# Optimization experiments

Measured on AMD Instinct MI355X. Metric: run time of the kernel, lower is better.

The kernel has to match this reference:

```python
import jax, jax.numpy as jnp
import numpy as np

N_NODES = 50000
N_EDGES = 800000
IN_DIM = 128
EDGE_DIM = 16
HIDDEN = 128
N_LAYERS = 3
N_GRAPHS = 256
BN_EPS = 1e-5


def setup_inputs() -> dict:
    key = jax.random.key(0)
    ks = jax.random.split(key, 24)
    s = 0.05
    inp = {
        "x": jax.random.normal(ks[0], (N_NODES, IN_DIM), jnp.float32),
        "edge_index": jax.random.randint(ks[1], (2, N_EDGES), 0, N_NODES, jnp.int32),
        "edge_attr": jax.random.normal(ks[2], (N_EDGES, EDGE_DIM), jnp.float32),
        "batch": jnp.sort(jax.random.randint(ks[3], (N_NODES,), 0, N_GRAPHS, jnp.int32)),
        "n_graphs": N_GRAPHS,
        # input projection
        "lin_in_w": jax.random.normal(ks[4], (IN_DIM, HIDDEN), jnp.float32) * s,
        "lin_in_b": jnp.zeros((HIDDEN,), jnp.float32),
        # per-layer message MLP (stacked over layers)
        "msg_w1": jax.random.normal(ks[5], (N_LAYERS, HIDDEN + EDGE_DIM, HIDDEN), jnp.float32) * s,
        "msg_b1": jnp.zeros((N_LAYERS, HIDDEN), jnp.float32),
        "msg_w2": jax.random.normal(ks[6], (N_LAYERS, HIDDEN, HIDDEN), jnp.float32) * s,
        "msg_b2": jnp.zeros((N_LAYERS, HIDDEN), jnp.float32),
        # BatchNorm (eval mode: running stats)
        "bn_gamma": jnp.ones((N_LAYERS, HIDDEN), jnp.float32),
        "bn_beta": jnp.zeros((N_LAYERS, HIDDEN), jnp.float32),
        "bn_mean": jax.random.normal(ks[7], (N_LAYERS, HIDDEN), jnp.float32) * 0.01,
        "bn_var": jax.random.uniform(ks[8], (N_LAYERS, HIDDEN), jnp.float32, 0.5, 1.5),
        # GRUCell params (PyTorch layout: [3*H, H], gate order r,z,n)
        "gru_wih": jax.random.normal(ks[9], (N_LAYERS, 3 * HIDDEN, HIDDEN), jnp.float32) * s,
        "gru_whh": jax.random.normal(ks[10], (N_LAYERS, 3 * HIDDEN, HIDDEN), jnp.float32) * s,
        "gru_bih": jnp.zeros((N_LAYERS, 3 * HIDDEN), jnp.float32),
        "gru_bhh": jnp.zeros((N_LAYERS, 3 * HIDDEN), jnp.float32),
        # readout linear: [2H -> H]
        "ro_w": jax.random.normal(ks[11], (2 * HIDDEN, HIDDEN), jnp.float32) * s,
        "ro_b": jnp.zeros((HIDDEN,), jnp.float32),
    }
    return inp


def _gru_cell(x, h, wih, whh, bih, bhh):
    gi = x @ wih.T + bih  # [N, 3H]
    gh = h @ whh.T + bhh
    ir, iz, inn = jnp.split(gi, 3, axis=1)
    hr, hz, hn = jnp.split(gh, 3, axis=1)
    r = jax.nn.sigmoid(ir + hr)
    z = jax.nn.sigmoid(iz + hz)
    n = jnp.tanh(inn + r * hn)
    return (1.0 - z) * n + z * h


def reference(x, edge_index, edge_attr, batch, n_graphs,
              lin_in_w, lin_in_b, msg_w1, msg_b1, msg_w2, msg_b2,
              bn_gamma, bn_beta, bn_mean, bn_var,
              gru_wih, gru_whh, gru_bih, gru_bhh, ro_w, ro_b):
    h = jax.nn.relu(x @ lin_in_w + lin_in_b)  # [N, H]
    src, dst = edge_index[0], edge_index[1]
    n_nodes = h.shape[0]
    for l in range(N_LAYERS):
        m_in = jnp.concatenate([h[src], edge_attr], axis=1)  # [E, H+Ed]
        m = jax.nn.relu(m_in @ msg_w1[l] + msg_b1[l]) @ msg_w2[l] + msg_b2[l]  # [E, H]
        agg = jax.ops.segment_sum(m, dst, num_segments=n_nodes)  # scatter-add
        h_new = _gru_cell(agg, h, gru_wih[l], gru_whh[l], gru_bih[l], gru_bhh[l])
        bn = (h_new - bn_mean[l]) * jax.lax.rsqrt(bn_var[l] + BN_EPS) * bn_gamma[l] + bn_beta[l]
        h = h + bn  # dropout is identity in eval mode
    # readout: segment mean + segment max over graphs
    cnt = jax.ops.segment_sum(jnp.ones((n_nodes, 1), h.dtype), batch, num_segments=n_graphs)
    z_sum = jax.ops.segment_sum(h, batch, num_segments=n_graphs)
    z_mean = z_sum / jnp.maximum(cnt, 1.0)
    z_max = jax.ops.segment_max(h, batch, num_segments=n_graphs)
    z_max = jnp.where(cnt > 0, z_max, 0.0)  # empty graphs -> 0 (as in torch code)
    z = jax.nn.relu(jnp.concatenate([z_mean, z_max], axis=1) @ ro_w + ro_b)
    return z
```

## Files before the change

### kernel.cpp

```cpp
#include <hip/hip_runtime.h>
#include <math.h>

constexpr int NN = 50000;
constexpr int NE = 800000;
constexpr int H  = 128;
constexpr int ED = 16;
constexpr int NL = 3;
constexpr int NG = 256;
constexpr int NBINS = 50176;

typedef __attribute__((ext_vector_type(8))) short bf8;
typedef __attribute__((ext_vector_type(4))) float f32x4;

__device__ __forceinline__ unsigned short f2bf(float f) {
    unsigned u = __float_as_uint(f);
    unsigned r = (u + 0x7FFFu + ((u >> 16) & 1u)) >> 16;
    return (unsigned short)r;
}
__device__ __forceinline__ float bf2f(unsigned short b) {
    return __uint_as_float(((unsigned)b) << 16);
}

__global__ __launch_bounds__(256) void k_zero4(float4* __restrict__ a, int n4) {
    int i = blockIdx.x * 256 + threadIdx.x;
    if (i < n4) a[i] = make_float4(0.f, 0.f, 0.f, 0.f);
}

__global__ __launch_bounds__(256) void k_sort_zero(int* __restrict__ counts) {
    int i = blockIdx.x * 256 + threadIdx.x;
    counts[i] = 0;
}

__global__ __launch_bounds__(256) void k_hist(const int* __restrict__ ei,
                                              int* __restrict__ counts) {
    int e = blockIdx.x * 256 + threadIdx.x;
    if (e < NE) atomicAdd(&counts[ei[NE + e]], 1);
}

__global__ __launch_bounds__(256) void k_scan1(const int* __restrict__ counts,
                                               int* __restrict__ incl,
                                               int* __restrict__ bsum) {
    __shared__ int s[256];
    int t = threadIdx.x;
    int i = blockIdx.x * 256 + t;
    int v = counts[i];
    s[t] = v;
    __syncthreads();
    #pragma unroll
    for (int off = 1; off < 256; off <<= 1) {
        int x = (t >= off) ? s[t - off] : 0;
        __syncthreads();
        s[t] += x;
        __syncthreads();
    }
    incl[i] = s[t];
    if (t == 255) bsum[blockIdx.x] = s[255];
}

__global__ __launch_bounds__(256) void k_scan2(int* __restrict__ bsum) {
    __shared__ int s[256];
    int t = threadIdx.x;
    int v = (t < 196) ? bsum[t] : 0;
    s[t] = v;
    __syncthreads();
    #pragma unroll
    for (int off = 1; off < 256; off <<= 1) {
        int x = (t >= off) ? s[t - off] : 0;
        __syncthreads();
        s[t] += x;
        __syncthreads();
    }
    if (t < 196) bsum[t] = s[t] - v;
}

__global__ __launch_bounds__(256) void k_scan3(const int* __restrict__ counts,
                                               const int* __restrict__ incl,
                                               const int* __restrict__ bsum,
                                               int* __restrict__ cur) {
    int i = blockIdx.x * 256 + threadIdx.x;
    cur[i] = incl[i] - counts[i] + bsum[blockIdx.x];
}

__global__ __launch_bounds__(256) void k_scatter_perm(const int* __restrict__ ei,
                                                      int* __restrict__ cur,
                                                      int* __restrict__ perm) {
    int e = blockIdx.x * 256 + threadIdx.x;
    if (e < NE) {
        int d = ei[NE + e];
        int pos = atomicAdd(&cur[d], 1);
        perm[pos] = e;
    }
}

__global__ __launch_bounds__(256) void k_prep(const float* __restrict__ wih,
                                              const float* __restrict__ whh,
                                              const float* __restrict__ w1,
                                              const float* __restrict__ w2,
                                              const float* __restrict__ lin_w,
                                              unsigned short* __restrict__ wgru,
                                              unsigned short* __restrict__ w1et,
                                              unsigned short* __restrict__ w2t,
                                              unsigned short* __restrict__ w1ht,
                                              unsigned short* __restrict__ winT) {
    int i = blockIdx.x * 256 + threadIdx.x;
    if (i < 294912) {
        int m = i / 147456, rem = i % 147456;
        wgru[i] = f2bf((m == 0 ? wih : whh)[rem]);
        return;
    }
    i -= 294912;
    if (i < NL * 128 * 32) {
        int l = i / 4096, rem = i % 4096;
        int n = rem >> 5, k = rem & 31;
        float v = (k < ED) ? w1[(size_t)l * 144 * 128 + (size_t)(128 + k) * 128 + n] : 0.f;
        w1et[i] = f2bf(v);
        return;
    }
    i -= NL * 128 * 32;
    if (i < NL * 128 * 128) {
        int l = i / 16384, rem = i % 16384;
        int n = rem >> 7, k = rem & 127;
        w2t[i] = f2bf(w2[(size_t)l * 16384 + (size_t)k * 128 + n]);
        return;
    }
    i -= NL * 128 * 128;
    if (i < NL * 128 * 128) {
        int l = i / 16384, rem = i % 16384;
        int n = rem >> 7, k = rem & 127;
        w1ht[i] = f2bf(w1[(size_t)l * 144 * 128 + (size_t)k * 128 + n]);
        return;
    }
    i -= NL * 128 * 128;
    if (i < 128 * 128) {
        int n = i >> 7, k = i & 127;
        winT[i] = f2bf(lin_w[k * 128 + n]);
    }
}

template <bool A_F32, bool RELU, bool BIAS, bool OUT_F32>
__global__ __launch_bounds__(256) void k_mfma_gemm(const float* __restrict__ A_f,
                                                   const unsigned short* __restrict__ A_bf,
                                                   const unsigned short* __restrict__ Bt,
                                                   const float* __restrict__ bias,
                                                   float* __restrict__ C_f,
                                                   unsigned short* __restrict__ C_bf,
                                                   int M) {
    __shared__ unsigned short As[32][136];
    const int t = threadIdx.x;
    const int w = t >> 6, lane = t & 63, l15 = lane & 15, q = lane >> 4;
    const int n0 = blockIdx.x * 32;

    bf8 bfr[2][4];
    #pragma unroll
    for (int nt = 0; nt < 2; ++nt) {
        int n = w * 32 + nt * 16 + l15;
        #pragma unroll
        for (int ks = 0; ks < 4; ++ks)
            bfr[nt][ks] = *(const bf8*)(Bt + (size_t)n * 128 + ks * 32 + q * 8);
    }

    {
        int r = t >> 3, cs = (t & 7) * 16;
        int row = n0 + r;
        union { uint4 u[2]; unsigned short s[16]; } pk;
        if (A_F32) {
            float4 v[4];
            if (row < M) {
                const float4* src = (const float4*)(A_f + (size_t)row * H + cs);
                v[0] = src[0]; v[1] = src[1]; v[2] = src[2]; v[3] = src[3];
            } else {
                v[0] = v[1] = v[2] = v[3] = make_float4(0.f, 0.f, 0.f, 0.f);
            }
            #pragma unroll
            for (int j = 0; j < 4; ++j) {
                pk.s[j * 4 + 0] = f2bf(v[j].x); pk.s[j * 4 + 1] = f2bf(v[j].y);
                pk.s[j * 4 + 2] = f2bf(v[j].z); pk.s[j * 4 + 3] = f2bf(v[j].w);
            }
        } else {
            if (row < M) {
                const uint4* src = (const uint4*)(A_bf + (size_t)row * H + cs);
                pk.u[0] = src[0]; pk.u[1] = src[1];
            } else {
                pk.u[0] = pk.u[1] = make_uint4(0, 0, 0, 0);
            }
        }
        *(uint4*)&As[r][cs] = pk.u[0];
        *(uint4*)&As[r][cs + 8] = pk.u[1];
    }
    __syncthreads();

    f32x4 acc[2][2];
    #pragma unroll
    for (int mt = 0; mt < 2; ++mt)
        #pragma unroll
        for (int nt = 0; nt < 2; ++nt) acc[mt][nt] = {0.f, 0.f, 0.f, 0.f};

    #pragma unroll
    for (int ks = 0; ks < 4; ++ks) {
        #pragma unroll
        for (int mt = 0; mt < 2; ++mt) {
            bf8 af = *(const bf8*)&As[mt * 16 + l15][ks * 32 + q * 8];
            acc[mt][0] = __builtin_amdgcn_mfma_f32_16x16x32_bf16(af, bfr[0][ks], acc[mt][0], 0, 0, 0);
            acc[mt][1] = __builtin_amdgcn_mfma_f32_16x16x32_bf16(af, bfr[1][ks], acc[mt][1], 0, 0, 0);
        }
    }

    #pragma unroll
    for (int nt = 0; nt < 2; ++nt) {
        int col = w * 32 + nt * 16 + l15;
        float bv = BIAS ? bias[col] : 0.f;
        #pragma unroll
        for (int mt = 0; mt < 2; ++mt) {
            #pragma unroll
            for (int r = 0; r < 4; ++r) {
                int node = n0 + mt * 16 + q * 4 + r;
                if (node < M) {
                    float v = acc[mt][nt][r] + bv;
                    if (RELU) v = fmaxf(v, 0.f);
                    if (OUT_F32) C_f[(size_t)node * H + col] = v;
                    C_bf[(size_t)node * H + col] = f2bf(v);
                }
            }
        }
    }
}

__global__ __launch_bounds__(256, 4) void k_edge_mfma(
        const unsigned short* __restrict__ p,
        const float* __restrict__ ea,
        const int* __restrict__ ei,
        const int* __restrict__ perm,
        const unsigned short* __restrict__ w1et,
        const float* __restrict__ b1,
        const unsigned short* __restrict__ w2t,
        const float* __restrict__ b2,
        float* __restrict__ agg) {
    __shared__ unsigned short hid_s[64][136];
    __shared__ unsigned short pm_s[64][136];
    __shared__ int src_s[64], dst_s[64], perm_s[64];

    const int t    = threadIdx.x;
    const int w    = t >> 6;
    const int lane = t & 63;
    const int l15  = lane & 15;
    const int q    = lane >> 4;

    bf8 w1f[2];
    bf8 w2f[2][4];
    float b1v[2], b2v[2];
    #pragma unroll
    for (int nt = 0; nt < 2; ++nt) {
        int n = w * 32 + nt * 16 + l15;
        w1f[nt] = *(const bf8*)(w1et + (size_t)n * 32 + q * 8);
        #pragma unroll
        for (int ks = 0; ks < 4; ++ks)
            w2f[nt][ks] = *(const bf8*)(w2t + (size_t)n * 128 + ks * 32 + q * 8);
        b1v[nt] = b1[n];
        b2v[nt] = b2[n];
    }

    const f32x4 zero = {0.f, 0.f, 0.f, 0.f};

    for (int base = blockIdx.x * 64; base < NE; base += gridDim.x * 64) {
        if (t < 64) {
            int e = perm[base + t];
            perm_s[t] = e;
            src_s[t]  = ei[e];
            dst_s[t]  = ei[NE + e];
        }
        __syncthreads();

        {
            int row = t >> 4, seg = t & 15;
            #pragma unroll
            for (int it = 0; it < 4; ++it, row += 16)
                *(uint4*)&pm_s[row][seg * 8] =
                    *(const uint4*)(p + (size_t)src_s[row] * H + seg * 8);
        }

        f32x4 acc1[4][2];
        #pragma unroll
        for (int mt = 0; mt < 4; ++mt) {
            bf8 af = {0, 0, 0, 0, 0, 0, 0, 0};
            if (q < 2) {
                int e = perm_s[mt * 16 + l15];
                const float4* e4 = (const float4*)(ea + (size_t)e * ED + q * 8);
                float4 v0 = e4[0], v1 = e4[1];
                af[0] = (short)f2bf(v0.x); af[1] = (short)f2bf(v0.y);
                af[2] = (short)f2bf(v0.z); af[3] = (short)f2bf(v0.w);
                af[4] = (short)f2bf(v1.x); af[5] = (short)f2bf(v1.y);
                af[6] = (short)f2bf(v1.z); af[7] = (short)f2bf(v1.w);
            }
            #pragma unroll
            for (int nt = 0; nt < 2; ++nt)
                acc1[mt][nt] = __builtin_amdgcn_mfma_f32_16x16x32_bf16(af, w1f[nt], zero, 0, 0, 0);
        }
        __syncthreads();

        #pragma unroll
        for (int mt = 0; mt < 4; ++mt) {
            #pragma unroll
            for (int r = 0; r < 4; ++r) {
                int er = mt * 16 + q * 4 + r;
                #pragma unroll
                for (int nt = 0; nt < 2; ++nt) {
                    int col = w * 32 + nt * 16 + l15;
                    float v = acc1[mt][nt][r] + bf2f(pm_s[er][col]) + b1v[nt];
                    hid_s[er][col] = f2bf(fmaxf(v, 0.f));
                }
            }
        }
        __syncthreads();

        f32x4 acc2[4][2];
        #pragma unroll
        for (int mt = 0; mt < 4; ++mt)
            #pragma unroll
            for (int nt = 0; nt < 2; ++nt) acc2[mt][nt] = zero;

        #pragma unroll
        for (int ks = 0; ks < 4; ++ks) {
            #pragma unroll
            for (int mt = 0; mt < 4; ++mt) {
                bf8 af = *(const bf8*)&hid_s[mt * 16 + l15][ks * 32 + q * 8];
                acc2[mt][0] = __builtin_amdgcn_mfma_f32_16x16x32_bf16(af, w2f[0][ks], acc2[mt][0], 0, 0, 0);
                acc2[mt][1] = __builtin_amdgcn_mfma_f32_16x16x32_bf16(af, w2f[1][ks], acc2[mt][1], 0, 0, 0);
            }
        }
        #pragma unroll
        for (int mt = 0; mt < 4; ++mt) {
            #pragma unroll
            for (int r = 0; r < 4; ++r) {
                int er = mt * 16 + q * 4 + r;
                #pragma unroll
                for (int nt = 0; nt < 2; ++nt) {
                    int col = w * 32 + nt * 16 + l15;
                    pm_s[er][col] = f2bf(acc2[mt][nt][r] + b2v[nt]);
                }
            }
        }
        __syncthreads();

        {
            int c = t & 127, hh = t >> 7;
            float sum = 0.f;
            int prev = dst_s[hh * 32];
            #pragma unroll 4
            for (int i = 0; i < 32; ++i) {
                int e = hh * 32 + i;
                int d = dst_s[e];
                float v = bf2f(pm_s[e][c]);
                if (d != prev) {
                    atomicAdd(&agg[(size_t)prev * H + c], sum);
                    sum = 0.f;
                    prev = d;
                }
                sum += v;
            }
            atomicAdd(&agg[(size_t)prev * H + c], sum);
        }
        __syncthreads();
    }
}

__device__ __forceinline__ float sigmoidf_(float x) { return 1.f / (1.f + expf(-x)); }

__global__ __launch_bounds__(256) void k_gru_mfma(const float* __restrict__ agg,
                                                  float* __restrict__ h,
                                                  unsigned short* __restrict__ h_bf,
                                                  const unsigned short* __restrict__ wih,
                                                  const unsigned short* __restrict__ whh,
                                                  const float* __restrict__ bih,
                                                  const float* __restrict__ bhh,
                                                  const float* __restrict__ gamma,
                                                  const float* __restrict__ beta,
                                                  const float* __restrict__ mean,
                                                  const float* __restrict__ var) {
    __shared__ unsigned short ab[32][136];
    __shared__ unsigned short hb[32][136];
    __shared__ float hf[32][132];
    const int t = threadIdx.x;
    const int w = t >> 6, lane = t & 63, l15 = lane & 15, q = lane >> 4;
    const int n0 = blockIdx.x * 32;

    {
        int r = t >> 3, cs = (t & 7) * 16;
        int row = n0 + r;
        float4 va[4], vh[4];
        if (row < NN) {
            const float4* sa = (const float4*)(agg + (size_t)row * H + cs);
            const float4* sh = (const float4*)(h + (size_t)row * H + cs);
            #pragma unroll
            for (int j = 0; j < 4; ++j) { va[j] = sa[j]; vh[j] = sh[j]; }
        } else {
            #pragma unroll
            for (int j = 0; j < 4; ++j) {
                va[j] = make_float4(0.f, 0.f, 0.f, 0.f);
                vh[j] = va[j];
            }
        }
        union { uint4 u[2]; unsigned short s[16]; } pa, ph;
        #pragma unroll
        for (int j = 0; j < 4; ++j) {
            pa.s[j * 4 + 0] = f2bf(va[j].x); pa.s[j * 4 + 1] = f2bf(va[j].y);
            pa.s[j * 4 + 2] = f2bf(va[j].z); pa.s[j * 4 + 3] = f2bf(va[j].w);
            ph.s[j * 4 + 0] = f2bf(vh[j].x); ph.s[j * 4 + 1] = f2bf(vh[j].y);
            ph.s[j * 4 + 2] = f2bf(vh[j].z); ph.s[j * 4 + 3] = f2bf(vh[j].w);
            *(float4*)&hf[r][cs + j * 4] = vh[j];
        }
        *(uint4*)&ab[r][cs] = pa.u[0];  *(uint4*)&ab[r][cs + 8] = pa.u[1];
        *(uint4*)&hb[r][cs] = ph.u[0];  *(uint4*)&hb[r][cs + 8] = ph.u[1];
    }
    __syncthreads();

    f32x4 acc[2][2][3][2];
    #pragma unroll
    for (int mt = 0; mt < 2; ++mt)
        #pragma unroll
        for (int io = 0; io < 2; ++io)
            #pragma unroll
            for (int g = 0; g < 3; ++g)
                #pragma unroll
                for (int nt = 0; nt < 2; ++nt) acc[mt][io][g][nt] = {0.f, 0.f, 0.f, 0.f};

    #pragma unroll
    for (int ks = 0; ks < 4; ++ks) {
        bf8 a_a[2], a_h[2];
        #pragma unroll
        for (int mt = 0; mt < 2; ++mt) {
            a_a[mt] = *(const bf8*)&ab[mt * 16 + l15][ks * 32 + q * 8];
            a_h[mt] = *(const bf8*)&hb[mt * 16 + l15][ks * 32 + q * 8];
        }
        #pragma unroll
        for (int g = 0; g < 3; ++g) {
            #pragma unroll
            for (int nt = 0; nt < 2; ++nt) {
                int n = g * 128 + w * 32 + nt * 16 + l15;
                bf8 bi = *(const bf8*)(wih + (size_t)n * 128 + ks * 32 + q * 8);
                bf8 bh = *(const bf8*)(whh + (size_t)n * 128 + ks * 32 + q * 8);
                #pragma unroll
                for (int mt = 0; mt < 2; ++mt) {
                    acc[mt][0][g][nt] = __builtin_amdgcn_mfma_f32_16x16x32_bf16(a_a[mt], bi, acc[mt][0][g][nt], 0, 0, 0);
                    acc[mt][1][g][nt] = __builtin_amdgcn_mfma_f32_16x16x32_bf16(a_h[mt], bh, acc[mt][1][g][nt], 0, 0, 0);
                }
            }
        }
    }

    #pragma unroll
    for (int nt = 0; nt < 2; ++nt) {
        int col = w * 32 + nt * 16 + l15;
        float bir = bih[col], biz = bih[128 + col], bin = bih[256 + col];
        float bhr = bhh[col], bhz = bhh[128 + col], bhn = bhh[256 + col];
        float ga = gamma[col], be = beta[col], mu = mean[col];
        float iv = rsqrtf(var[col] + 1e-5f);
        #pragma unroll
        for (int mt = 0; mt < 2; ++mt) {
            #pragma unroll
            for (int r = 0; r < 4; ++r) {
                int nl = mt * 16 + q * 4 + r;
                int node = n0 + nl;
                if (node < NN) {
                    float ir = acc[mt][0][0][nt][r] + bir;
                    float iz = acc[mt][0][1][nt][r] + biz;
                    float in = acc[mt][0][2][nt][r] + bin;
                    float hr = acc[mt][1][0][nt][r] + bhr;
                    float hz = acc[mt][1][1][nt][r] + bhz;
                    float hn = acc[mt][1][2][nt][r] + bhn;
                    float rg = sigmoidf_(ir + hr);
                    float zg = sigmoidf_(iz + hz);
                    float ng = tanhf(in + rg * hn);
                    float hv = hf[nl][col];
                    float hnew = (1.f - zg) * ng + zg * hv;
                    float bn = (hnew - mu) * iv * ga + be;
                    float out = hv + bn;
                    h[(size_t)node * H + col] = out;
                    h_bf[(size_t)node * H + col] = f2bf(out);
                }
            }
        }
    }
}

__device__ __forceinline__ unsigned fkey(float f) {
    unsigned b = __float_as_uint(f);
    return (b & 0x80000000u) ? ~b : (b | 0x80000000u);
}
__device__ __forceinline__ float funkey(unsigned k) {
    unsigned b = (k & 0x80000000u) ? (k & 0x7FFFFFFFu) : ~k;
    return __uint_as_float(b);
}

__global__ __launch_bounds__(256) void k_ro_init(float* __restrict__ gsum,
                                                 unsigned* __restrict__ gmaxb,
                                                 float* __restrict__ gcnt) {
    int i = blockIdx.x * 256 + threadIdx.x;
    if (i < NG * H) { gsum[i] = 0.f; gmaxb[i] = 0u; }
    if (i < NG) gcnt[i] = 0.f;
}

__global__ __launch_bounds__(256) void k_ro_scan(const float* __restrict__ h,
                                                 const int* __restrict__ batch,
                                                 float* __restrict__ gsum,
                                                 unsigned* __restrict__ gmaxb,
                                                 float* __restrict__ gcnt) {
    __shared__ int bt_s[64];
    const int t = threadIdx.x;
    const int n0 = blockIdx.x * 64;
    if (t < 64) bt_s[t] = (n0 + t < NN) ? batch[n0 + t] : -1;
    __syncthreads();

    int c = t & 127, hh = t >> 7;
    float sum = 0.f, mx = -3.4e38f, cnt = 0.f;
    int prev = bt_s[hh * 32];
    #pragma unroll 4
    for (int i = 0; i < 32; ++i) {
        int e = hh * 32 + i;
        int g = bt_s[e];
        if (g != prev) {
            if (prev >= 0) {
                atomicAdd(&gsum[prev * H + c], sum);
                atomicMax(&gmaxb[prev * H + c], fkey(mx));
                if (c == 0) atomicAdd(&gcnt[prev], cnt);
            }
            sum = 0.f; mx = -3.4e38f; cnt = 0.f;
            prev = g;
        }
        if (g >= 0) {
            float v = h[(size_t)(n0 + e) * H + c];
            sum += v;
            mx = fmaxf(mx, v);
            cnt += 1.f;
        }
    }
    if (prev >= 0) {
        atomicAdd(&gsum[prev * H + c], sum);
        atomicMax(&gmaxb[prev * H + c], fkey(mx));
        if (c == 0) atomicAdd(&gcnt[prev], cnt);
    }
}

__global__ __launch_bounds__(128) void k_ro_final(const float* __restrict__ gsum,
                                                  const unsigned* __restrict__ gmaxb,
                                                  const float* __restrict__ gcnt,
                                                  const float* __restrict__ row,
                                                  const float* __restrict__ rob,
                                                  float* __restrict__ out) {
    __shared__ float cat[256];
    const int g = blockIdx.x, t = threadIdx.x;
    float cnt = gcnt[g];
    float inv = 1.f / fmaxf(cnt, 1.f);
    cat[t] = gsum[g * H + t] * inv;
    float mx = funkey(gmaxb[g * H + t]);
    cat[128 + t] = (cnt > 0.f) ? mx : 0.f;
    __syncthreads();
    float acc = rob[t];
    #pragma unroll 4
    for (int k = 0; k < 256; ++k) acc += cat[k] * row[k * H + t];
    out[g * H + t] = fmaxf(acc, 0.f);
}

extern "C" void kernel_launch(void* const* d_in, const int* in_sizes, int n_in,
                              void* d_out, int out_size, void* d_ws, size_t ws_size,
                              hipStream_t stream) {
    const float* x        = (const float*)d_in[0];
    const int*   ei       = (const int*)d_in[1];
    const float* ea       = (const float*)d_in[2];
    const int*   batch    = (const int*)d_in[3];
    const float* lin_in_w = (const float*)d_in[5];
    const float* lin_in_b = (const float*)d_in[6];
    const float* msg_w1   = (const float*)d_in[7];
    const float* msg_b1   = (const float*)d_in[8];
    const float* msg_w2   = (const float*)d_in[9];
    const float* msg_b2   = (const float*)d_in[10];
    const float* bn_gamma = (const float*)d_in[11];
    const float* bn_beta  = (const float*)d_in[12];
    const float* bn_mean  = (const float*)d_in[13];
    const float* bn_var   = (const float*)d_in[14];
    const float* gru_wih  = (const float*)d_in[15];
    const float* gru_whh  = (const float*)d_in[16];
    const float* gru_bih  = (const float*)d_in[17];
    const float* gru_bhh  = (const float*)d_in[18];
    const float* ro_w     = (const float*)d_in[19];
    const float* ro_b     = (const float*)d_in[20];

    float* ws = (float*)d_ws;
    float*          h     = ws;
    float*          agg   = ws + 6400000;
    unsigned short* h_bf  = (unsigned short*)(ws + 12800000);
    unsigned short* p_bf  = (unsigned short*)(ws + 16000000);
    float*          gsum  = ws + 19200000;
    unsigned*       gmaxb = (unsigned*)(ws + 19232768);
    float*          gcnt  = ws + 19265536;
    unsigned short* wgru  = (unsigned short*)(ws + 19265792);
    unsigned short* w1et  = (unsigned short*)(ws + 19413248);
    unsigned short* w2t   = (unsigned short*)(ws + 19419392);
    unsigned short* w1ht  = (unsigned short*)(ws + 19443968);
    unsigned short* winT  = (unsigned short*)(ws + 19468544);
    int*            cnts  = (int*)(ws + 19476736);
    int*            incl  = (int*)(ws + 19526912);
    int*            cur   = (int*)(ws + 19577088);
    int*            bsum  = (int*)(ws + 19627264);
    int*            perm  = (int*)(ws + 19627520);

    k_prep<<<1648, 256, 0, stream>>>(gru_wih, gru_whh, msg_w1, msg_w2, lin_in_w,
                                     wgru, w1et, w2t, w1ht, winT);

    k_sort_zero<<<196, 256, 0, stream>>>(cnts);
    k_hist<<<3125, 256, 0, stream>>>(ei, cnts);
    k_scan1<<<196, 256, 0, stream>>>(cnts, incl, bsum);
    k_scan2<<<1, 256, 0, stream>>>(bsum);
    k_scan3<<<196, 256, 0, stream>>>(cnts, incl, bsum, cur);
    k_scatter_perm<<<3125, 256, 0, stream>>>(ei, cur, perm);

    k_mfma_gemm<true, true, true, true><<<1563, 256, 0, stream>>>(
        x, nullptr, winT, lin_in_b, h, h_bf, NN);

    for (int l = 0; l < NL; ++l) {
        k_mfma_gemm<false, false, false, false><<<1563, 256, 0, stream>>>(
            nullptr, h_bf, w1ht + (size_t)l * 16384, nullptr, nullptr, p_bf, NN);
        k_zero4<<<6250, 256, 0, stream>>>((float4*)agg, 1600000);
        k_edge_mfma<<<1024, 256, 0, stream>>>(p_bf, ea, ei, perm,
                                              w1et + (size_t)l * 4096, msg_b1 + l * 128,
                                              w2t + (size_t)l * 16384, msg_b2 + l * 128,
                                              agg);
        k_gru_mfma<<<1563, 256, 0, stream>>>(agg, h, h_bf,
                                             wgru + (size_t)l * 49152,
                                             wgru + (size_t)(NL + l) * 49152,
                                             gru_bih + l * 384, gru_bhh + l * 384,
                                             bn_gamma + l * 128, bn_beta + l * 128,
                                             bn_mean + l * 128, bn_var + l * 128);
    }

    k_ro_init<<<128, 256, 0, stream>>>(gsum, gmaxb, gcnt);
    k_ro_scan<<<782, 256, 0, stream>>>(h, batch, gsum, gmaxb, gcnt);
    k_ro_final<<<NG, 128, 0, stream>>>(gsum, gmaxb, gcnt, ro_w, ro_b, (float*)d_out);
}
```

Baseline: 862.9 us.

## Pre-gather sorted src/dst and bf16 edge attrs; shrink edge kernel LDS

Adds a one-time gather that writes src and dst indices plus bf16 edge attributes in dst-sorted order. The per-layer edge kernel then reads them contiguously instead of doing indirect perm lookups and fp32 conversion. The edge kernel reuses a single LDS buffer (with an extra barrier), which allows higher occupancy (launch bounds 6, more blocks). It also drops the bf16 copy of h, so the GEMM converts from fp32 itself, and replaces the zeroing kernels with hipMemsetAsync. The cost is an extra preprocessing pass and one more sync per tile.

```diff
diff --git a/kernel.cpp b/kernel.cpp
--- a/kernel.cpp
+++ b/kernel.cpp
@@ -7,7 +7,6 @@
 constexpr int ED = 16;
 constexpr int NL = 3;
 constexpr int NG = 256;
-constexpr int NBINS = 50176;
 
 typedef __attribute__((ext_vector_type(8))) short bf8;
 typedef __attribute__((ext_vector_type(4))) float f32x4;
@@ -19,11 +18,6 @@
 }
 __device__ __forceinline__ float bf2f(unsigned short b) {
     return __uint_as_float(((unsigned)b) << 16);
-}
-
-__global__ __launch_bounds__(256) void k_zero4(float4* __restrict__ a, int n4) {
-    int i = blockIdx.x * 256 + threadIdx.x;
-    if (i < n4) a[i] = make_float4(0.f, 0.f, 0.f, 0.f);
 }
 
 __global__ __launch_bounds__(256) void k_sort_zero(int* __restrict__ counts) {
@@ -90,6 +84,31 @@
         int pos = atomicAdd(&cur[d], 1);
         perm[pos] = e;
     }
+}
+
+__global__ __launch_bounds__(256) void k_gather(const int* __restrict__ ei,
+                                                const float* __restrict__ ea,
+                                                int* __restrict__ perm,
+                                                int* __restrict__ dsts,
+                                                unsigned short* __restrict__ ea_bf) {
+    int i = blockIdx.x * 256 + threadIdx.x;
+    if (i >= NE) return;
+    int e = perm[i];
+    perm[i] = ei[e];
+    dsts[i] = ei[NE + e];
+    const float4* s = (const float4*)(ea + (size_t)e * ED);
+    float4 v[4];
+    #pragma unroll
+    for (int j = 0; j < 4; ++j) v[j] = s[j];
+    union { uint4 u[2]; unsigned short sh[16]; } pk;
+    #pragma unroll
+    for (int j = 0; j < 4; ++j) {
+        pk.sh[j * 4 + 0] = f2bf(v[j].x); pk.sh[j * 4 + 1] = f2bf(v[j].y);
+        pk.sh[j * 4 + 2] = f2bf(v[j].z); pk.sh[j * 4 + 3] = f2bf(v[j].w);
+    }
+    uint4* d = (uint4*)(ea_bf + (size_t)i * 16);
+    d[0] = pk.u[0];
+    d[1] = pk.u[1];
 }
 
 __global__ __launch_bounds__(256) void k_prep(const float* __restrict__ wih,
@@ -137,9 +156,8 @@
     }
 }
 
-template <bool A_F32, bool RELU, bool BIAS, bool OUT_F32>
-__global__ __launch_bounds__(256) void k_mfma_gemm(const float* __restrict__ A_f,
-                                                   const unsigned short* __restrict__ A_bf,
+template <bool RELU, bool BIAS, bool OUT_F32, bool OUT_BF>
+__global__ __launch_bounds__(256) void k_mfma_gemm(const float* __restrict__ A,
                                                    const unsigned short* __restrict__ Bt,
                                                    const float* __restrict__ bias,
                                                    float* __restrict__ C_f,
@@ -162,27 +180,20 @@
     {
         int r = t >> 3, cs = (t & 7) * 16;
         int row = n0 + r;
+        float4 v[4];
+        if (row < M) {
+            const float4* src = (const float4*)(A + (size_t)row * H + cs);
+            #pragma unroll
+            for (int j = 0; j < 4; ++j) v[j] = src[j];
+        } else {
+            #pragma unroll
+            for (int j = 0; j < 4; ++j) v[j] = make_float4(0.f, 0.f, 0.f, 0.f);
+        }
         union { uint4 u[2]; unsigned short s[16]; } pk;
-        if (A_F32) {
-            float4 v[4];
-            if (row < M) {
-                const float4* src = (const float4*)(A_f + (size_t)row * H + cs);
-                v[0] = src[0]; v[1] = src[1]; v[2] = src[2]; v[3] = src[3];
-            } else {
-                v[0] = v[1] = v[2] = v[3] = make_float4(0.f, 0.f, 0.f, 0.f);
-            }
-            #pragma unroll
-            for (int j = 0; j < 4; ++j) {
-                pk.s[j * 4 + 0] = f2bf(v[j].x); pk.s[j * 4 + 1] = f2bf(v[j].y);
-                pk.s[j * 4 + 2] = f2bf(v[j].z); pk.s[j * 4 + 3] = f2bf(v[j].w);
-            }
-        } else {
-            if (row < M) {
-                const uint4* src = (const uint4*)(A_bf + (size_t)row * H + cs);
-                pk.u[0] = src[0]; pk.u[1] = src[1];
-            } else {
-                pk.u[0] = pk.u[1] = make_uint4(0, 0, 0, 0);
-            }
+        #pragma unroll
+        for (int j = 0; j < 4; ++j) {
+            pk.s[j * 4 + 0] = f2bf(v[j].x); pk.s[j * 4 + 1] = f2bf(v[j].y);
+            pk.s[j * 4 + 2] = f2bf(v[j].z); pk.s[j * 4 + 3] = f2bf(v[j].w);
         }
         *(uint4*)&As[r][cs] = pk.u[0];
         *(uint4*)&As[r][cs + 8] = pk.u[1];
@@ -218,26 +229,25 @@
                     float v = acc[mt][nt][r] + bv;
                     if (RELU) v = fmaxf(v, 0.f);
                     if (OUT_F32) C_f[(size_t)node * H + col] = v;
-                    C_bf[(size_t)node * H + col] = f2bf(v);
+                    if (OUT_BF)  C_bf[(size_t)node * H + col] = f2bf(v);
                 }
             }
         }
     }
 }
 
-__global__ __launch_bounds__(256, 4) void k_edge_mfma(
+__global__ __launch_bounds__(256, 6) void k_edge_mfma(
         const unsigned short* __restrict__ p,
-        const float* __restrict__ ea,
-        const int* __restrict__ ei,
-        const int* __restrict__ perm,
+        const int* __restrict__ srcs,
+        const int* __restrict__ dsts,
+        const unsigned short* __restrict__ ea_bf,
         const unsigned short* __restrict__ w1et,
         const float* __restrict__ b1,
         const unsigned short* __restrict__ w2t,
         const float* __restrict__ b2,
         float* __restrict__ agg) {
-    __shared__ unsigned short hid_s[64][136];
-    __shared__ unsigned short pm_s[64][136];
-    __shared__ int src_s[64], dst_s[64], perm_s[64];
+    __shared__ unsigned short u_s[64][136];
+    __shared__ int src_s[64], dst_s[64];
 
     const int t    = threadIdx.x;
     const int w    = t >> 6;
@@ -262,35 +272,26 @@
     const f32x4 zero = {0.f, 0.f, 0.f, 0.f};
 
     for (int base = blockIdx.x * 64; base < NE; base += gridDim.x * 64) {
-        if (t < 64) {
-            int e = perm[base + t];
-            perm_s[t] = e;
-            src_s[t]  = ei[e];
-            dst_s[t]  = ei[NE + e];
-        }
+        if (t < 64)       src_s[t] = srcs[base + t];
+        else if (t < 128) dst_s[t - 64] = dsts[base + t - 64];
         __syncthreads();
 
         {
             int row = t >> 4, seg = t & 15;
             #pragma unroll
-            for (int it = 0; it < 4; ++it, row += 16)
-                *(uint4*)&pm_s[row][seg * 8] =
-                    *(const uint4*)(p + (size_t)src_s[row] * H + seg * 8);
+            for (int it = 0; it < 4; ++it) {
+                int rr = row + 16 * it;
+                *(uint4*)&u_s[rr][seg * 8] =
+                    *(const uint4*)(p + (size_t)src_s[rr] * H + seg * 8);
+            }
         }
 
         f32x4 acc1[4][2];
         #pragma unroll
         for (int mt = 0; mt < 4; ++mt) {
             bf8 af = {0, 0, 0, 0, 0, 0, 0, 0};
-            if (q < 2) {
-                int e = perm_s[mt * 16 + l15];
-                const float4* e4 = (const float4*)(ea + (size_t)e * ED + q * 8);
-                float4 v0 = e4[0], v1 = e4[1];
-                af[0] = (short)f2bf(v0.x); af[1] = (short)f2bf(v0.y);
-                af[2] = (short)f2bf(v0.z); af[3] = (short)f2bf(v0.w);
-                af[4] = (short)f2bf(v1.x); af[5] = (short)f2bf(v1.y);
-                af[6] = (short)f2bf(v1.z); af[7] = (short)f2bf(v1.w);
-            }
+            if (q < 2)
+                af = *(const bf8*)(ea_bf + (size_t)(base + mt * 16 + l15) * 16 + q * 8);
             #pragma unroll
             for (int nt = 0; nt < 2; ++nt)
                 acc1[mt][nt] = __builtin_amdgcn_mfma_f32_16x16x32_bf16(af, w1f[nt], zero, 0, 0, 0);
@@ -305,8 +306,8 @@
                 #pragma unroll
                 for (int nt = 0; nt < 2; ++nt) {
                     int col = w * 32 + nt * 16 + l15;
-                    float v = acc1[mt][nt][r] + bf2f(pm_s[er][col]) + b1v[nt];
-                    hid_s[er][col] = f2bf(fmaxf(v, 0.f));
+                    float v = acc1[mt][nt][r] + bf2f(u_s[er][col]) + b1v[nt];
+                    u_s[er][col] = f2bf(fmaxf(v, 0.f));
                 }
             }
         }
@@ -322,11 +323,13 @@
         for (int ks = 0; ks < 4; ++ks) {
             #pragma unroll
             for (int mt = 0; mt < 4; ++mt) {
-                bf8 af = *(const bf8*)&hid_s[mt * 16 + l15][ks * 32 + q * 8];
+                bf8 af = *(const bf8*)&u_s[mt * 16 + l15][ks * 32 + q * 8];
                 acc2[mt][0] = __builtin_amdgcn_mfma_f32_16x16x32_bf16(af, w2f[0][ks], acc2[mt][0], 0, 0, 0);
                 acc2[mt][1] = __builtin_amdgcn_mfma_f32_16x16x32_bf16(af, w2f[1][ks], acc2[mt][1], 0, 0, 0);
             }
         }
+        __syncthreads();
+
         #pragma unroll
         for (int mt = 0; mt < 4; ++mt) {
             #pragma unroll
@@ -335,7 +338,7 @@
                 #pragma unroll
                 for (int nt = 0; nt < 2; ++nt) {
                     int col = w * 32 + nt * 16 + l15;
-                    pm_s[er][col] = f2bf(acc2[mt][nt][r] + b2v[nt]);
+                    u_s[er][col] = f2bf(acc2[mt][nt][r] + b2v[nt]);
                 }
             }
         }
@@ -349,7 +352,7 @@
             for (int i = 0; i < 32; ++i) {
                 int e = hh * 32 + i;
                 int d = dst_s[e];
-                float v = bf2f(pm_s[e][c]);
+                float v = bf2f(u_s[e][c]);
                 if (d != prev) {
                     atomicAdd(&agg[(size_t)prev * H + c], sum);
                     sum = 0.f;
@@ -367,7 +370,6 @@
 
 __global__ __launch_bounds__(256) void k_gru_mfma(const float* __restrict__ agg,
                                                   float* __restrict__ h,
-                                                  unsigned short* __restrict__ h_bf,
                                                   const unsigned short* __restrict__ wih,
                                                   const unsigned short* __restrict__ whh,
                                                   const float* __restrict__ bih,
@@ -473,9 +475,7 @@
                     float hv = hf[nl][col];
                     float hnew = (1.f - zg) * ng + zg * hv;
                     float bn = (hnew - mu) * iv * ga + be;
-                    float out = hv + bn;
-                    h[(size_t)node * H + col] = out;
-                    h_bf[(size_t)node * H + col] = f2bf(out);
+                    h[(size_t)node * H + col] = hv + bn;
                 }
             }
         }
@@ -489,14 +489,6 @@
 __device__ __forceinline__ float funkey(unsigned k) {
     unsigned b = (k & 0x80000000u) ? (k & 0x7FFFFFFFu) : ~k;
     return __uint_as_float(b);
-}
-
-__global__ __launch_bounds__(256) void k_ro_init(float* __restrict__ gsum,
-                                                 unsigned* __restrict__ gmaxb,
-                                                 float* __restrict__ gcnt) {
-    int i = blockIdx.x * 256 + threadIdx.x;
-    if (i < NG * H) { gsum[i] = 0.f; gmaxb[i] = 0u; }
-    if (i < NG) gcnt[i] = 0.f;
 }
 
 __global__ __launch_bounds__(256) void k_ro_scan(const float* __restrict__ h,
@@ -587,21 +579,22 @@
     float* ws = (float*)d_ws;
     float*          h     = ws;
     float*          agg   = ws + 6400000;
-    unsigned short* h_bf  = (unsigned short*)(ws + 12800000);
-    unsigned short* p_bf  = (unsigned short*)(ws + 16000000);
-    float*          gsum  = ws + 19200000;
-    unsigned*       gmaxb = (unsigned*)(ws + 19232768);
-    float*          gcnt  = ws + 19265536;
-    unsigned short* wgru  = (unsigned short*)(ws + 19265792);
-    unsigned short* w1et  = (unsigned short*)(ws + 19413248);
-    unsigned short* w2t   = (unsigned short*)(ws + 19419392);
-    unsigned short* w1ht  = (unsigned short*)(ws + 19443968);
-    unsigned short* winT  = (unsigned short*)(ws + 19468544);
-    int*            cnts  = (int*)(ws + 19476736);
-    int*            incl  = (int*)(ws + 19526912);
-    int*            cur   = (int*)(ws + 19577088);
-    int*            bsum  = (int*)(ws + 19627264);
-    int*            perm  = (int*)(ws + 19627520);
+    unsigned short* p_bf  = (unsigned short*)(ws + 12800000);
+    float*          gsum  = ws + 16000000;
+    unsigned*       gmaxb = (unsigned*)(ws + 16032768);
+    float*          gcnt  = ws + 16065536;
+    unsigned short* wgru  = (unsigned short*)(ws + 16065792);
+    unsigned short* w1et  = (unsigned short*)(ws + 16213248);
+    unsigned short* w2t   = (unsigned short*)(ws + 16219392);
+    unsigned short* w1ht  = (unsigned short*)(ws + 16243968);
+    unsigned short* winT  = (unsigned short*)(ws + 16268544);
+    int*            cnts  = (int*)(ws + 16276736);
+    int*            incl  = (int*)(ws + 16326912);
+    int*            cur   = (int*)(ws + 16377088);
+    int*            bsum  = (int*)(ws + 16427264);
+    int*            srcs  = (int*)(ws + 16427520);
+    int*            dsts  = (int*)(ws + 17227520);
+    unsigned short* ea_bf = (unsigned short*)(ws + 18027520);
 
     k_prep<<<1648, 256, 0, stream>>>(gru_wih, gru_whh, msg_w1, msg_w2, lin_in_w,
                                      wgru, w1et, w2t, w1ht, winT);
@@ -611,20 +604,21 @@
     k_scan1<<<196, 256, 0, stream>>>(cnts, incl, bsum);
     k_scan2<<<1, 256, 0, stream>>>(bsum);
     k_scan3<<<196, 256, 0, stream>>>(cnts, incl, bsum, cur);
-    k_scatter_perm<<<3125, 256, 0, stream>>>(ei, cur, perm);
-
-    k_mfma_gemm<true, true, true, true><<<1563, 256, 0, stream>>>(
-        x, nullptr, winT, lin_in_b, h, h_bf, NN);
+    k_scatter_perm<<<3125, 256, 0, stream>>>(ei, cur, srcs);
+    k_gather<<<3125, 256, 0, stream>>>(ei, ea, srcs, dsts, ea_bf);
+
+    k_mfma_gemm<true, true, true, false><<<1563, 256, 0, stream>>>(
+        x, winT, lin_in_b, h, nullptr, NN);
 
     for (int l = 0; l < NL; ++l) {
-        k_mfma_gemm<false, false, false, false><<<1563, 256, 0, stream>>>(
-            nullptr, h_bf, w1ht + (size_t)l * 16384, nullptr, nullptr, p_bf, NN);
-        k_zero4<<<6250, 256, 0, stream>>>((float4*)agg, 1600000);
-        k_edge_mfma<<<1024, 256, 0, stream>>>(p_bf, ea, ei, perm,
+        k_mfma_gemm<false, false, false, true><<<1563, 256, 0, stream>>>(
+            h, w1ht + (size_t)l * 16384, nullptr, nullptr, p_bf, NN);
+        hipMemsetAsync(agg, 0, (size_t)NN * H * sizeof(float), stream);
+        k_edge_mfma<<<1536, 256, 0, stream>>>(p_bf, srcs, dsts, ea_bf,
                                               w1et + (size_t)l * 4096, msg_b1 + l * 128,
                                               w2t + (size_t)l * 16384, msg_b2 + l * 128,
                                               agg);
-        k_gru_mfma<<<1563, 256, 0, stream>>>(agg, h, h_bf,
+        k_gru_mfma<<<1563, 256, 0, stream>>>(agg, h,
                                              wgru + (size_t)l * 49152,
                                              wgru + (size_t)(NL + l) * 49152,
                                              gru_bih + l * 384, gru_bhh + l * 384,
@@ -632,7 +626,7 @@
                                              bn_mean + l * 128, bn_var + l * 128);
     }
 
-    k_ro_init<<<128, 256, 0, stream>>>(gsum, gmaxb, gcnt);
+    hipMemsetAsync(gsum, 0, (size_t)(NG * H * 2 + NG) * sizeof(float), stream);
     k_ro_scan<<<782, 256, 0, stream>>>(h, batch, gsum, gmaxb, gcnt);
     k_ro_final<<<NG, 128, 0, stream>>>(gsum, gmaxb, gcnt, ro_w, ro_b, (float*)d_out);
 }
```

Measured after the change: 964.7 us. +11.8%, slower.
